# Optimization experiments

Measured on AMD Instinct MI355X. Metric: run time of the kernel, lower is better.

Reference implementation:

```python
import jax, jax.numpy as jnp
import numpy as np
import math

N, LQ, C = 4, 5440, 256
H, L, P = 8, 4, 4
D = C // H
SHAPES = [(64, 64), (32, 32), (16, 16), (8, 8)]
STARTS = [0, 4096, 5120, 5376]
LEN_IN = 5440


def setup_inputs() -> dict:
    key = jax.random.key(0)
    ks = jax.random.split(key, 12)
    s = 1.0 / math.sqrt(C)
    return {
        "query": jax.random.normal(ks[0], (N, LQ, C), jnp.float32),
        "reference_points": jax.random.uniform(ks[1], (N, LQ, L, 2), jnp.float32),
        "input_flatten": jax.random.normal(ks[2], (N, LEN_IN, C), jnp.float32),
        "input_spatial_shapes": jnp.asarray(SHAPES, jnp.int32),
        "input_level_start_index": jnp.asarray(STARTS, jnp.int32),
        "w_off": jax.random.normal(ks[3], (C, H * L * P * 2), jnp.float32) * 0.01,
        "b_off": jax.random.normal(ks[4], (H * L * P * 2,), jnp.float32) * 0.5,
        "w_attn": jax.random.normal(ks[5], (C, H * L * P), jnp.float32) * 0.01,
        "b_attn": jnp.zeros((H * L * P,), jnp.float32),
        "w_val": jax.random.normal(ks[6], (C, C), jnp.float32) * s,
        "b_val": jnp.zeros((C,), jnp.float32),
        "w_out": jax.random.normal(ks[7], (C, C), jnp.float32) * s,
        "b_out": jnp.zeros((C,), jnp.float32),
    }


def _gather_corner(lv, yi, xi, w):
    # lv: (N, h*w, H, D); yi, xi: (N, Lq, H, P) int32 -> (N, Lq, H, P, D)
    n, lq, h_, p_ = yi.shape
    idx = yi * w + xi
    idx2 = idx.transpose(0, 1, 3, 2).reshape(n, lq * p_, h_)[..., None]
    g = jnp.take_along_axis(lv, idx2, axis=1)  # (N, Lq*P, H, D)
    return g.reshape(n, lq, p_, h_, -1).transpose(0, 1, 3, 2, 4)


def _msdeform(query, reference_points, input_flatten, shapes, starts,
              w_off, b_off, w_attn, b_attn, w_val, b_val, w_out, b_out):
    n, lq, c = query.shape
    value = (input_flatten @ w_val + b_val).reshape(n, -1, H, D)
    off = (query @ w_off + b_off).reshape(n, lq, H, L, P, 2)
    attn = jax.nn.softmax((query @ w_attn + b_attn).reshape(n, lq, H, L * P), axis=-1)
    # sampling locations in [0,1], (N, Lq, H, L, P, 2)
    loc = jnp.clip(reference_points[:, :, None, :, None, :] + off, 0.0, 1.0)
    sampled = []
    for lvl, (hh, ww) in enumerate(shapes):
        s0 = starts[lvl]
        lv = value[:, s0:s0 + hh * ww]  # (N, hh*ww, H, D)
        xy = loc[:, :, :, lvl] * jnp.asarray([ww, hh], jnp.float32) - 0.5  # (N,Lq,H,P,2)
        x, y = xy[..., 0], xy[..., 1]
        x0 = jnp.floor(x)
        y0 = jnp.floor(y)
        x0i = jnp.clip(x0.astype(jnp.int32), 0, ww - 1)
        x1i = jnp.clip(x0.astype(jnp.int32) + 1, 0, ww - 1)
        y0i = jnp.clip(y0.astype(jnp.int32), 0, hh - 1)
        y1i = jnp.clip(y0.astype(jnp.int32) + 1, 0, hh - 1)
        x0f, x1f = x0i.astype(x.dtype), x1i.astype(x.dtype)
        y0f, y1f = y0i.astype(y.dtype), y1i.astype(y.dtype)
        wa = ((x1f - x) * (y1f - y))[..., None]
        wb = ((x1f - x) * (y - y0f))[..., None]
        wc = ((x - x0f) * (y1f - y))[..., None]
        wd = ((x - x0f) * (y - y0f))[..., None]
        va = _gather_corner(lv, y0i, x0i, ww)
        vb = _gather_corner(lv, y1i, x0i, ww)
        vc = _gather_corner(lv, y0i, x1i, ww)
        vd = _gather_corner(lv, y1i, x1i, ww)
        sampled.append(wa * va + wb * vb + wc * vc + wd * vd)
    sampled = jnp.concatenate(sampled, axis=3)  # (N, Lq, H, L*P, D)
    out = jnp.einsum('nqhp,nqhpd->nqhd', attn, sampled).reshape(n, lq, c)
    return out @ w_out + b_out


def reference(query, reference_points, input_flatten, input_spatial_shapes,
              input_level_start_index, w_off, b_off, w_attn, b_attn,
              w_val, b_val, w_out, b_out):
    shapes = [tuple(int(v) for v in row) for row in np.asarray(input_spatial_shapes)]
    starts = [int(v) for v in np.asarray(input_level_start_index)]
    return _msdeform(query, reference_points, input_flatten, shapes, starts,
                     w_off, b_off, w_attn, b_attn, w_val, b_val, w_out, b_out)
```

## Files before the change

kernel.cpp:

```cpp
#include <hip/hip_runtime.h>
#include <hip/hip_fp16.h>
#include <math.h>

#define C_DIM 256
#define H_DIM 8
#define L_DIM 4
#define P_DIM 4
#define LQ 5440
#define LEN_IN 5440
#define NB 4
#define M_ROWS (NB * LQ)
#define NPANEL (M_ROWS / 128)

typedef __attribute__((ext_vector_type(8))) _Float16 f16x8;
typedef __attribute__((ext_vector_type(8))) unsigned short u16x8;
typedef __attribute__((ext_vector_type(4))) float f32x4;

__device__ __forceinline__ void split_f32(float a, __half& h, __half& l) {
    h = __float2half(a);
    l = __float2half(a - __half2float(h));
}

__global__ __launch_bounds__(256) void convert_all(const float* __restrict__ w_val,
                                                   const float* __restrict__ w_off,
                                                   const float* __restrict__ w_attn,
                                                   const float* __restrict__ w_out,
                                                   const float* __restrict__ b_off,
                                                   const float* __restrict__ b_attn,
                                                   __half* __restrict__ wv_hi, __half* __restrict__ wv_lo,
                                                   __half* __restrict__ wc_hi, __half* __restrict__ wc_lo,
                                                   __half* __restrict__ wt_hi, __half* __restrict__ wt_lo,
                                                   float* __restrict__ bc) {
    const int b = blockIdx.x, k = threadIdx.x;
    if (b < 896) {
        const float* w; __half *hi, *lo; int ncols, col, orow;
        if (b < 256)      { w = w_val;  hi = wv_hi; lo = wv_lo; ncols = 256; col = b;       orow = col; }
        else if (b < 512) { w = w_off;  hi = wc_hi; lo = wc_lo; ncols = 256; col = b - 256; orow = col; }
        else if (b < 640) { w = w_attn; hi = wc_hi; lo = wc_lo; ncols = 128; col = b - 512; orow = col + 256; }
        else              { w = w_out;  hi = wt_hi; lo = wt_lo; ncols = 256; col = b - 640; orow = col; }
        const float a = w[(size_t)k * ncols + col];
        __half h, l;
        split_f32(a, h, l);
        hi[(size_t)orow * 256 + k] = h;
        lo[(size_t)orow * 256 + k] = l;
    } else if (b == 896) {
        bc[k] = b_off[k];
    } else {
        if (k < 128) bc[256 + k] = b_attn[k];
    }
}

__global__ __launch_bounds__(256, 4) void gemm_f16x3(
    int split,
    const float* __restrict__ A0, const __half* __restrict__ B0h, const __half* __restrict__ B0l,
    const float* __restrict__ bias0, float* __restrict__ out0, int NC0,
    const float* __restrict__ A1, const __half* __restrict__ B1h, const __half* __restrict__ B1l,
    const float* __restrict__ bias1, float* __restrict__ out1, int NC1) {
    __shared__ __align__(16) __half sA[2][128][32];
    __shared__ __align__(16) __half sB[2][64][32];
    __shared__ __align__(16) float sepi[4][16][32];

    const int bid = blockIdx.x;
    const float* A; const __half* Bhi; const __half* Blo;
    const float* bias; float* outp; int NC, idx;
    if (bid < split) { A = A0; Bhi = B0h; Blo = B0l; bias = bias0; outp = out0; NC = NC0; idx = bid; }
    else             { A = A1; Bhi = B1h; Blo = B1l; bias = bias1; outp = out1; NC = NC1; idx = bid - split; }
    const int NX = NC >> 6;
    const int y = idx / NX;
    const int x = idx - y * NX;

    const int n0 = x * 64;
    const int row0 = y * 128;
    const int t = threadIdx.x;
    const int w = t >> 6, lane = t & 63;
    const int bm = (w >> 1) * 64, bn = (w & 1) * 32;
    const int fr = lane & 15;
    const int fc = lane >> 4;

    const int ar1 = t >> 2, ar2 = ar1 + 64;
    const int ak8 = t & 3;
    const int asw1 = (ak8 ^ ((ar1 >> 1) & 3)) * 8;
    const int asw2 = (ak8 ^ ((ar2 >> 1) & 3)) * 8;
    const int br = t >> 2;
    const int bc8 = t & 3;
    const int bsw = (bc8 ^ ((br >> 1) & 3)) * 8;

    const size_t ga1 = (size_t)(row0 + ar1) * 256 + ak8 * 8;
    const size_t ga2 = (size_t)(row0 + ar2) * 256 + ak8 * 8;
    const size_t gb  = (size_t)(n0 + br) * 256 + bc8 * 8;

    f32x4 acc[4][2];
#pragma unroll
    for (int m = 0; m < 4; ++m)
#pragma unroll
        for (int n = 0; n < 2; ++n)
#pragma unroll
            for (int r = 0; r < 4; ++r) acc[m][n][r] = 0.f;

    float4 pa[4];
    float4 pb[2];
    pa[0] = *(const float4*)(A + ga1);
    pa[1] = *(const float4*)(A + ga1 + 4);
    pa[2] = *(const float4*)(A + ga2);
    pa[3] = *(const float4*)(A + ga2 + 4);
    pb[0] = *(const float4*)(Bhi + gb);
    pb[1] = *(const float4*)(Blo + gb);

    for (int kt = 0; kt < 8; ++kt) {
        if (kt) __syncthreads();
#pragma unroll
        for (int ch = 0; ch < 2; ++ch) {
            const float4 u = pa[2 * ch], v = pa[2 * ch + 1];
            const float e[8] = {u.x, u.y, u.z, u.w, v.x, v.y, v.z, v.w};
            u16x8 Hh, Ll;
#pragma unroll
            for (int i = 0; i < 8; ++i) {
                __half h, l;
                split_f32(e[i], h, l);
                Hh[i] = __half_as_ushort(h);
                Ll[i] = __half_as_ushort(l);
            }
            const int row = ch ? ar2 : ar1;
            const int sw = ch ? asw2 : asw1;
            *(u16x8*)&sA[0][row][sw] = Hh;
            *(u16x8*)&sA[1][row][sw] = Ll;
        }
        *(float4*)&sB[0][br][bsw] = pb[0];
        *(float4*)&sB[1][br][bsw] = pb[1];
        __syncthreads();
        if (kt < 7) {
            const size_t ko = (size_t)(kt + 1) * 32;
            pa[0] = *(const float4*)(A + ga1 + ko);
            pa[1] = *(const float4*)(A + ga1 + ko + 4);
            pa[2] = *(const float4*)(A + ga2 + ko);
            pa[3] = *(const float4*)(A + ga2 + ko + 4);
            pb[0] = *(const float4*)(Bhi + gb + ko);
            pb[1] = *(const float4*)(Blo + gb + ko);
        }

        f16x8 bhf[2], blf[2];
#pragma unroll
        for (int n = 0; n < 2; ++n) {
            const int rowb = bn + n * 16 + fr;
            const int swb = (fc ^ ((rowb >> 1) & 3)) * 8;
            bhf[n] = *(const f16x8*)&sB[0][rowb][swb];
            blf[n] = *(const f16x8*)&sB[1][rowb][swb];
        }
#pragma unroll
        for (int m = 0; m < 4; ++m) {
            const int rowa = bm + m * 16 + fr;
            const int swa = (fc ^ ((rowa >> 1) & 3)) * 8;
            const f16x8 ah = *(const f16x8*)&sA[0][rowa][swa];
            const f16x8 al = *(const f16x8*)&sA[1][rowa][swa];
#pragma unroll
            for (int n = 0; n < 2; ++n) {
                acc[m][n] = __builtin_amdgcn_mfma_f32_16x16x32_f16(ah, bhf[n], acc[m][n], 0, 0, 0);
                acc[m][n] = __builtin_amdgcn_mfma_f32_16x16x32_f16(al, bhf[n], acc[m][n], 0, 0, 0);
                acc[m][n] = __builtin_amdgcn_mfma_f32_16x16x32_f16(ah, blf[n], acc[m][n], 0, 0, 0);
            }
        }
    }

    float bv[2];
#pragma unroll
    for (int n = 0; n < 2; ++n) bv[n] = bias[n0 + bn + n * 16 + fr];

#pragma unroll
    for (int m = 0; m < 4; ++m) {
#pragma unroll
        for (int n = 0; n < 2; ++n) {
            const int kch = n * 4 + (fr >> 2);
            const int lo4 = fr & 3;
#pragma unroll
            for (int r = 0; r < 4; ++r) {
                const int rw = fc * 4 + r;
                const int sk = (kch ^ (rw & 7)) & 7;
                sepi[w][rw][sk * 4 + lo4] = acc[m][n][r] + bv[n];
            }
        }
#pragma unroll
        for (int jj = 0; jj < 2; ++jj) {
            const int flat = jj * 64 + lane;
            const int rw = flat >> 3;
            const int k = flat & 7;
            const int sk = (k ^ (rw & 7)) & 7;
            const float4 vv = *(const float4*)&sepi[w][rw][sk * 4];
            const int grow = row0 + bm + m * 16 + rw;
            *(float4*)&outp[(size_t)grow * NC + (n0 + bn + k * 4)] = vv;
        }
    }
}

__global__ __launch_bounds__(256) void sample_kernel(const float* __restrict__ value,
                                                     const float* __restrict__ ol,
                                                     const float* __restrict__ refpts,
                                                     float* __restrict__ tmp) {
    const int t = threadIdx.x;
    const int w = t >> 6, lane = t & 63;

    __shared__ __align__(16) float4 s_aw[4][128];
    __shared__ __align__(16) uint4 s_of[4][128];

    const int h = lane >> 3;
    const unsigned l16 = (unsigned)(lane * 16);

    const int bid = blockIdx.x;
    const int xcd = bid & 7;
    const int pos = bid >> 3;
    const int n = xcd >> 1;
    const int qgrp = (xcd & 1) * 340 + pos;

    const char* vbn = (const char*)value + (size_t)n * (LEN_IN * C_DIM * 4);

    for (int it = 0; it < 2; ++it) {
        const int q = n * LQ + qgrp * 8 + w * 2 + it;

#pragma unroll
        for (int s = 0; s < 2; ++s) {
            const int j = lane + 64 * s;
            const int hq = j >> 4, lp = j & 15;
            const int l = lp >> 2;
            const int ww = 64 >> l;
            int st = 0;
            if (l == 1) st = 4096;
            else if (l == 2) st = 5120;
            else if (l == 3) st = 5376;

            const float2 oxy = *(const float2*)&ol[(size_t)q * 384 + 2 * j];
            const float2 rxy = *(const float2*)&refpts[((size_t)q * L_DIM + l) * 2];

            const float fw = (float)ww;
            const float x = fminf(fmaxf(rxy.x + oxy.x, 0.f), 1.f) * fw - 0.5f;
            const float y = fminf(fmaxf(rxy.y + oxy.y, 0.f), 1.f) * fw - 0.5f;
            const int xi = (int)floorf(x);
            const int yi = (int)floorf(y);
            const int x0i = min(max(xi, 0), ww - 1);
            const int x1i = min(max(xi + 1, 0), ww - 1);
            const int y0i = min(max(yi, 0), ww - 1);
            const int y1i = min(max(yi + 1, 0), ww - 1);
            const float wx0 = (float)x1i - x, wx1 = x - (float)x0i;
            const float wy0 = (float)y1i - y, wy1 = y - (float)y0i;

            const float lg = ol[(size_t)q * 384 + 256 + j];
            float m = lg;
#pragma unroll
            for (int o = 8; o; o >>= 1) m = fmaxf(m, __shfl_xor(m, o, 16));
            const float e = expf(lg - m);
            float sm = e;
#pragma unroll
            for (int o = 8; o; o >>= 1) sm += __shfl_xor(sm, o, 16);
            const float a = e / sm;

            const int p = lp * 8 + (hq ^ (lp & 7));
            float4 aw;
            aw.x = a * (wx0 * wy0);
            aw.y = a * (wx0 * wy1);
            aw.z = a * (wx1 * wy0);
            aw.w = a * (wx1 * wy1);
            uint4 of;
            of.x = (unsigned)(st + y0i * ww + x0i) << 10;
            of.y = (unsigned)(st + y1i * ww + x0i) << 10;
            of.z = (unsigned)(st + y0i * ww + x1i) << 10;
            of.w = (unsigned)(st + y1i * ww + x1i) << 10;
            s_aw[w][p] = aw;
            s_of[w][p] = of;
        }

        float4 acc;
        acc.x = 0.f; acc.y = 0.f; acc.z = 0.f; acc.w = 0.f;
#pragma unroll
        for (int lp = 0; lp < 16; ++lp) {
            const int p = lp * 8 + (h ^ (lp & 7));
            const float4 aw = s_aw[w][p];
            const uint4 of = s_of[w][p];
            const float4 v0 = *(const float4*)(vbn + (of.x + l16));
            const float4 v1 = *(const float4*)(vbn + (of.y + l16));
            const float4 v2 = *(const float4*)(vbn + (of.z + l16));
            const float4 v3 = *(const float4*)(vbn + (of.w + l16));
            acc.x += aw.x * v0.x + aw.y * v1.x + aw.z * v2.x + aw.w * v3.x;
            acc.y += aw.x * v0.y + aw.y * v1.y + aw.z * v2.y + aw.w * v3.y;
            acc.z += aw.x * v0.z + aw.y * v1.z + aw.z * v2.z + aw.w * v3.z;
            acc.w += aw.x * v0.w + aw.y * v1.w + aw.z * v2.w + aw.w * v3.w;
        }
        *(float4*)&tmp[(size_t)q * 256 + (size_t)(lane * 4)] = acc;
    }
}

extern "C" void kernel_launch(void* const* d_in, const int* in_sizes, int n_in,
                              void* d_out, int out_size, void* d_ws, size_t ws_size,
                              hipStream_t stream) {
    const float* query         = (const float*)d_in[0];
    const float* refpts        = (const float*)d_in[1];
    const float* input_flatten = (const float*)d_in[2];
    const float* w_off  = (const float*)d_in[5];
    const float* b_off  = (const float*)d_in[6];
    const float* w_attn = (const float*)d_in[7];
    const float* b_attn = (const float*)d_in[8];
    const float* w_val  = (const float*)d_in[9];
    const float* b_val  = (const float*)d_in[10];
    const float* w_out  = (const float*)d_in[11];
    const float* b_out  = (const float*)d_in[12];
    float* out = (float*)d_out;

    const size_t nr = (size_t)M_ROWS;
    float* p = (float*)d_ws;
    float* value_ws = p; p += nr * 256;
    float* ol_ws    = p; p += nr * 384;
    float* tmp_ws   = p; p += nr * 256;
    float* bc_ws    = p; p += 384;
    __half* wv_hi = (__half*)p;
    __half* wv_lo = wv_hi + 256 * 256;
    __half* wc_hi = wv_lo + 256 * 256;
    __half* wc_lo = wc_hi + 384 * 256;
    __half* wt_hi = wc_lo + 384 * 256;
    __half* wt_lo = wt_hi + 256 * 256;

    convert_all<<<898, 256, 0, stream>>>(w_val, w_off, w_attn, w_out, b_off, b_attn,
                                         wv_hi, wv_lo, wc_hi, wc_lo, wt_hi, wt_lo, bc_ws);

    const int GV = NPANEL * 4;
    const int GO = NPANEL * 6;

    gemm_f16x3<<<GV + GO, 256, 0, stream>>>(GV,
        input_flatten, wv_hi, wv_lo, b_val, value_ws, 256,
        query, wc_hi, wc_lo, bc_ws, ol_ws, 384);

    sample_kernel<<<M_ROWS / 8, 256, 0, stream>>>(value_ws, ol_ws, refpts, tmp_ws);

    gemm_f16x3<<<GV, 256, 0, stream>>>(GV,
        tmp_ws, wt_hi, wt_lo, b_out, out, 256,
        tmp_ws, wt_hi, wt_lo, b_out, out, 256);
}
```

Baseline: 141.7 us.

## Shrink GEMM tile to 64 rows, template on width, swizzle block order

Halves the GEMM M-tile from 128 to 64 rows, so each block computes a 64x64 output with a 2x2 MFMA fragment grid per wave. The column count becomes a template parameter. Blocks are remapped so that 8 consecutive block ids cover 8 different row panels at the same column tile, which should improve L2 reuse of the weight tile. The combined value/offset GEMM launch is split into two separate launches. Smaller tiles give more blocks and better occupancy but less A/B reuse per block, plus one extra launch.

After: 172.7 us. +21.9%, slower.

```diff
diff --git a/kernel.cpp b/kernel.cpp
--- a/kernel.cpp
+++ b/kernel.cpp
@@ -10,7 +10,7 @@
 #define LEN_IN 5440
 #define NB 4
 #define M_ROWS (NB * LQ)
-#define NPANEL (M_ROWS / 128)
+#define NPANEL64 (M_ROWS / 64)
 
 typedef __attribute__((ext_vector_type(8))) _Float16 f16x8;
 typedef __attribute__((ext_vector_type(8))) unsigned short u16x8;
@@ -50,67 +50,62 @@
     }
 }
 
-__global__ __launch_bounds__(256, 4) void gemm_f16x3(
-    int split,
-    const float* __restrict__ A0, const __half* __restrict__ B0h, const __half* __restrict__ B0l,
-    const float* __restrict__ bias0, float* __restrict__ out0, int NC0,
-    const float* __restrict__ A1, const __half* __restrict__ B1h, const __half* __restrict__ B1l,
-    const float* __restrict__ bias1, float* __restrict__ out1, int NC1) {
-    __shared__ __align__(16) __half sA[2][128][32];
+template <int NC>
+__global__ __launch_bounds__(256, 4) void gemm_f16x3(const float* __restrict__ A,
+                                                     const __half* __restrict__ Bhi,
+                                                     const __half* __restrict__ Blo,
+                                                     const float* __restrict__ bias,
+                                                     float* __restrict__ outp) {
+    constexpr int NX = NC / 64;
+
+    __shared__ __align__(16) __half sA[2][64][32];
     __shared__ __align__(16) __half sB[2][64][32];
     __shared__ __align__(16) float sepi[4][16][32];
 
     const int bid = blockIdx.x;
-    const float* A; const __half* Bhi; const __half* Blo;
-    const float* bias; float* outp; int NC, idx;
-    if (bid < split) { A = A0; Bhi = B0h; Blo = B0l; bias = bias0; outp = out0; NC = NC0; idx = bid; }
-    else             { A = A1; Bhi = B1h; Blo = B1l; bias = bias1; outp = out1; NC = NC1; idx = bid - split; }
-    const int NX = NC >> 6;
-    const int y = idx / NX;
-    const int x = idx - y * NX;
+    const int c = bid & 7;
+    const int rest = bid >> 3;
+    const int x = rest % NX;
+    const int yg = rest / NX;
+    const int y = yg * 8 + c;
+    if (y >= NPANEL64) return;
 
     const int n0 = x * 64;
-    const int row0 = y * 128;
+    const int row0 = y * 64;
     const int t = threadIdx.x;
     const int w = t >> 6, lane = t & 63;
-    const int bm = (w >> 1) * 64, bn = (w & 1) * 32;
+    const int bm = (w >> 1) * 32, bn = (w & 1) * 32;
     const int fr = lane & 15;
     const int fc = lane >> 4;
 
-    const int ar1 = t >> 2, ar2 = ar1 + 64;
+    const int ar = t >> 2;
     const int ak8 = t & 3;
-    const int asw1 = (ak8 ^ ((ar1 >> 1) & 3)) * 8;
-    const int asw2 = (ak8 ^ ((ar2 >> 1) & 3)) * 8;
+    const int asw = (ak8 ^ ((ar >> 1) & 3)) * 8;
     const int br = t >> 2;
     const int bc8 = t & 3;
     const int bsw = (bc8 ^ ((br >> 1) & 3)) * 8;
 
-    const size_t ga1 = (size_t)(row0 + ar1) * 256 + ak8 * 8;
-    const size_t ga2 = (size_t)(row0 + ar2) * 256 + ak8 * 8;
-    const size_t gb  = (size_t)(n0 + br) * 256 + bc8 * 8;
-
-    f32x4 acc[4][2];
-#pragma unroll
-    for (int m = 0; m < 4; ++m)
+    const size_t ga = (size_t)(row0 + ar) * 256 + ak8 * 8;
+    const size_t gb = (size_t)(n0 + br) * 256 + bc8 * 8;
+
+    f32x4 acc[2][2];
+#pragma unroll
+    for (int m = 0; m < 2; ++m)
 #pragma unroll
         for (int n = 0; n < 2; ++n)
 #pragma unroll
             for (int r = 0; r < 4; ++r) acc[m][n][r] = 0.f;
 
-    float4 pa[4];
-    float4 pb[2];
-    pa[0] = *(const float4*)(A + ga1);
-    pa[1] = *(const float4*)(A + ga1 + 4);
-    pa[2] = *(const float4*)(A + ga2);
-    pa[3] = *(const float4*)(A + ga2 + 4);
+    float4 pa[2], pb[2];
+    pa[0] = *(const float4*)(A + ga);
+    pa[1] = *(const float4*)(A + ga + 4);
     pb[0] = *(const float4*)(Bhi + gb);
     pb[1] = *(const float4*)(Blo + gb);
 
     for (int kt = 0; kt < 8; ++kt) {
         if (kt) __syncthreads();
-#pragma unroll
-        for (int ch = 0; ch < 2; ++ch) {
-            const float4 u = pa[2 * ch], v = pa[2 * ch + 1];
+        {
+            const float4 u = pa[0], v = pa[1];
             const float e[8] = {u.x, u.y, u.z, u.w, v.x, v.y, v.z, v.w};
             u16x8 Hh, Ll;
 #pragma unroll
@@ -120,20 +115,16 @@
                 Hh[i] = __half_as_ushort(h);
                 Ll[i] = __half_as_ushort(l);
             }
-            const int row = ch ? ar2 : ar1;
-            const int sw = ch ? asw2 : asw1;
-            *(u16x8*)&sA[0][row][sw] = Hh;
-            *(u16x8*)&sA[1][row][sw] = Ll;
+            *(u16x8*)&sA[0][ar][asw] = Hh;
+            *(u16x8*)&sA[1][ar][asw] = Ll;
         }
         *(float4*)&sB[0][br][bsw] = pb[0];
         *(float4*)&sB[1][br][bsw] = pb[1];
         __syncthreads();
         if (kt < 7) {
             const size_t ko = (size_t)(kt + 1) * 32;
-            pa[0] = *(const float4*)(A + ga1 + ko);
-            pa[1] = *(const float4*)(A + ga1 + ko + 4);
-            pa[2] = *(const float4*)(A + ga2 + ko);
-            pa[3] = *(const float4*)(A + ga2 + ko + 4);
+            pa[0] = *(const float4*)(A + ga + ko);
+            pa[1] = *(const float4*)(A + ga + ko + 4);
             pb[0] = *(const float4*)(Bhi + gb + ko);
             pb[1] = *(const float4*)(Blo + gb + ko);
         }
@@ -147,7 +138,7 @@
             blf[n] = *(const f16x8*)&sB[1][rowb][swb];
         }
 #pragma unroll
-        for (int m = 0; m < 4; ++m) {
+        for (int m = 0; m < 2; ++m) {
             const int rowa = bm + m * 16 + fr;
             const int swa = (fc ^ ((rowa >> 1) & 3)) * 8;
             const f16x8 ah = *(const f16x8*)&sA[0][rowa][swa];
@@ -166,7 +157,7 @@
     for (int n = 0; n < 2; ++n) bv[n] = bias[n0 + bn + n * 16 + fr];
 
 #pragma unroll
-    for (int m = 0; m < 4; ++m) {
+    for (int m = 0; m < 2; ++m) {
 #pragma unroll
         for (int n = 0; n < 2; ++n) {
             const int kch = n * 4 + (fr >> 2);
@@ -318,16 +309,13 @@
     convert_all<<<898, 256, 0, stream>>>(w_val, w_off, w_attn, w_out, b_off, b_attn,
                                          wv_hi, wv_lo, wc_hi, wc_lo, wt_hi, wt_lo, bc_ws);
 
-    const int GV = NPANEL * 4;
-    const int GO = NPANEL * 6;
-
-    gemm_f16x3<<<GV + GO, 256, 0, stream>>>(GV,
-        input_flatten, wv_hi, wv_lo, b_val, value_ws, 256,
-        query, wc_hi, wc_lo, bc_ws, ol_ws, 384);
+    const int g256 = 8 * 4 * 43;
+    const int g384 = 8 * 6 * 43;
+
+    gemm_f16x3<256><<<g256, 256, 0, stream>>>(input_flatten, wv_hi, wv_lo, b_val, value_ws);
+    gemm_f16x3<384><<<g384, 256, 0, stream>>>(query, wc_hi, wc_lo, bc_ws, ol_ws);
 
     sample_kernel<<<M_ROWS / 8, 256, 0, stream>>>(value_ws, ol_ws, refpts, tmp_ws);
 
-    gemm_f16x3<<<GV, 256, 0, stream>>>(GV,
-        tmp_ws, wt_hi, wt_lo, b_out, out, 256,
-        tmp_ws, wt_hi, wt_lo, b_out, out, 256);
-}
+    gemm_f16x3<256><<<g256, 256, 0, stream>>>(tmp_ws, wt_hi, wt_lo, b_out, out);
+}
```
